# Optimization experiments

Measured on AMD Instinct MI355X. Metric: run time of the kernel, lower is better.

## Reference

```python
import jax, jax.numpy as jnp
import numpy as np

B, C, H, W = 4, 256, 180, 180
N_BOX = 64


def _box_mask(gt_boxes, H, W):
    # gt_boxes: [B, N, 4] int32 = [lt_x, lt_y, rb_x, rb_y]
    # Original fills gt_mask[i, lt_y:rb_y, rb_x:lt_x] = 1 (x-slice is flipped).
    ys = jnp.arange(H)[:, None]            # [H,1]
    xs = jnp.arange(W)[None, :]            # [1,W]
    lt_x = gt_boxes[:, :, 0][:, :, None, None]
    lt_y = gt_boxes[:, :, 1][:, :, None, None]
    rb_x = gt_boxes[:, :, 2][:, :, None, None]
    rb_y = gt_boxes[:, :, 3][:, :, None, None]
    inside = (ys >= lt_y) & (ys < rb_y) & (xs >= rb_x) & (xs < lt_x)  # [B,N,H,W]
    return jnp.any(inside, axis=1)         # [B,H,W] bool


def setup_inputs() -> dict:
    key = jax.random.key(0)
    k1, k2, k3, k4, k5, k6 = jax.random.split(key, 6)
    inp = jax.random.normal(k1, (B, C, H, W), dtype=jnp.float32)
    tgt = jax.random.normal(k2, (B, C, H, W), dtype=jnp.float32)
    # Build boxes with flipped-x convention: lt_x > rb_x, lt_y < rb_y.
    x2 = jax.random.randint(k3, (B, N_BOX), 0, W - 50)
    bw = jax.random.randint(k4, (B, N_BOX), 5, 45)
    y1 = jax.random.randint(k5, (B, N_BOX), 0, H - 50)
    bh = jax.random.randint(k6, (B, N_BOX), 5, 45)
    gt_boxes = jnp.stack([x2 + bw, y1, x2, y1 + bh], axis=-1).astype(jnp.int32)
    return {"input": inp, "target": tgt, "gt_boxes": gt_boxes}


def reference(input, target, gt_boxes):
    b, c, h, w = input.shape
    mask = _box_mask(gt_boxes, h, w)                        # [B,H,W]
    x = jnp.transpose(input, (0, 2, 3, 1))                  # [B,H,W,C]
    t = jnp.transpose(target, (0, 2, 3, 1))
    positives = jnp.any(t != 0, axis=-1).astype(x.dtype) * mask.astype(x.dtype)
    pos_normalizer = jnp.sum(positives)
    reg_weights = positives / pos_normalizer                # [B,H,W]
    # masked weighted MSE; zero weights make non-positive pixels contribute 0,
    # matching the original's boolean-index gather.
    t = jnp.where(jnp.isnan(t), x, t)
    loss = 0.5 * (x - t) ** 2 * reg_weights[..., None]      # [B,H,W,C]
    imitation_loss = jnp.sum(jnp.mean(loss, axis=-1)) / b
    return imitation_loss
```

## Files before the change

### kernel.cpp

```cpp
#include <hip/hip_runtime.h>
#include <hip/hip_bf16.h>

#define B_    4
#define C_    256
#define H_    180
#define W_    180
#define NBOX  64
#define HW_   (H_ * W_)
#define NPIX  (B_ * HW_)

__global__ __launch_bounds__(256) void mask_feat_loss_main(
    const float* __restrict__ x,
    const float* __restrict__ t,
    const int*   __restrict__ boxes,
    float*        ws_sum,
    unsigned int* ws_cnt)
{
    const int p = blockIdx.x * blockDim.x + threadIdx.x;

    float s = 0.0f;
    int   cnt = 0;

    if (p < NPIX) {
        const int b  = p / HW_;
        const int hw = p - b * HW_;
        const int h  = hw / W_;
        const int w  = hw - h * W_;

        bool mask = false;
        const int* bb = boxes + b * NBOX * 4;
        #pragma unroll 8
        for (int n = 0; n < NBOX; ++n) {
            const int ltx = bb[n * 4 + 0];
            const int lty = bb[n * 4 + 1];
            const int rbx = bb[n * 4 + 2];
            const int rby = bb[n * 4 + 3];
            mask |= ((h >= lty) & (h < rby) & (w >= rbx) & (w < ltx));
        }

        if (mask) {
            const float* xp = x + (size_t)b * C_ * HW_ + hw;
            const float* tp = t + (size_t)b * C_ * HW_ + hw;
            bool anynz = false;
            #pragma unroll 8
            for (int c = 0; c < C_; ++c) {
                const float tv = tp[(size_t)c * HW_];
                const float xv = xp[(size_t)c * HW_];
                anynz |= (tv != 0.0f);
                const float d = xv - tv;
                float term = 0.5f * d * d;
                if (isnan(tv)) term = 0.0f;
                s += term;
            }
            if (anynz) cnt = 1;
            else       s = 0.0f;
        }
    }

    #pragma unroll
    for (int off = 32; off > 0; off >>= 1) {
        s   += __shfl_down(s, off, 64);
        cnt += __shfl_down(cnt, off, 64);
    }

    __shared__ float ssum[4];
    __shared__ int   scnt[4];
    const int lane = threadIdx.x & 63;
    const int wid  = threadIdx.x >> 6;
    if (lane == 0) { ssum[wid] = s; scnt[wid] = cnt; }
    __syncthreads();

    if (threadIdx.x == 0) {
        const float S  = ssum[0] + ssum[1] + ssum[2] + ssum[3];
        const int   Cn = scnt[0] + scnt[1] + scnt[2] + scnt[3];
        if (S != 0.0f) atomicAdd(ws_sum, S);
        if (Cn != 0)   atomicAdd(ws_cnt, (unsigned int)Cn);
    }
}

__global__ void mask_feat_loss_finalize(const float* ws_sum,
                                        const unsigned int* ws_cnt,
                                        float* out)
{
    const float S = ws_sum[0];
    const float n = (float)ws_cnt[0];
    out[0] = S / (n * (float)C_ * (float)B_);
}

extern "C" void kernel_launch(void* const* d_in, const int* in_sizes, int n_in,
                              void* d_out, int out_size, void* d_ws, size_t ws_size,
                              hipStream_t stream)
{
    const float* x     = (const float*)d_in[0];
    const float* t     = (const float*)d_in[1];
    const int*   boxes = (const int*)d_in[2];
    float* out = (float*)d_out;

    float*        ws_sum = (float*)d_ws;
    unsigned int* ws_cnt = (unsigned int*)((char*)d_ws + sizeof(float));

    hipMemsetAsync(d_ws, 0, 2 * sizeof(unsigned int), stream);

    const int threads = 256;
    const int blocks  = (NPIX + threads - 1) / threads;
    mask_feat_loss_main<<<blocks, threads, 0, stream>>>(x, t, boxes, ws_sum, ws_cnt);
    mask_feat_loss_finalize<<<1, 1, 0, stream>>>(ws_sum, ws_cnt, out);
}
```

Measured before the change: 54.19 us.

## Split channel loop across four waves per pixel group

```diff
diff --git a/kernel.cpp b/kernel.cpp
--- a/kernel.cpp
+++ b/kernel.cpp
@@ -16,65 +16,66 @@
     float*        ws_sum,
     unsigned int* ws_cnt)
 {
-    const int p = blockIdx.x * blockDim.x + threadIdx.x;
+    const int lane = threadIdx.x & 63;
+    const int wid  = threadIdx.x >> 6;
+    const int p    = blockIdx.x * 64 + lane;
+
+    const int b  = p / HW_;
+    const int hw = p - b * HW_;
+    const int h  = hw / W_;
+    const int w  = hw - h * W_;
+
+    bool mask = false;
+    const int* bb = boxes + b * NBOX * 4;
+    #pragma unroll 8
+    for (int n = 0; n < NBOX; ++n) {
+        const int ltx = bb[n * 4 + 0];
+        const int lty = bb[n * 4 + 1];
+        const int rbx = bb[n * 4 + 2];
+        const int rby = bb[n * 4 + 3];
+        mask |= ((h >= lty) & (h < rby) & (w >= rbx) & (w < ltx));
+    }
 
     float s = 0.0f;
-    int   cnt = 0;
-
-    if (p < NPIX) {
-        const int b  = p / HW_;
-        const int hw = p - b * HW_;
-        const int h  = hw / W_;
-        const int w  = hw - h * W_;
-
-        bool mask = false;
-        const int* bb = boxes + b * NBOX * 4;
+    int   nz = 0;
+    if (mask) {
+        const size_t base = ((size_t)b * C_ + wid * 64) * HW_ + hw;
+        const float* xp = x + base;
+        const float* tp = t + base;
         #pragma unroll 8
-        for (int n = 0; n < NBOX; ++n) {
-            const int ltx = bb[n * 4 + 0];
-            const int lty = bb[n * 4 + 1];
-            const int rbx = bb[n * 4 + 2];
-            const int rby = bb[n * 4 + 3];
-            mask |= ((h >= lty) & (h < rby) & (w >= rbx) & (w < ltx));
-        }
-
-        if (mask) {
-            const float* xp = x + (size_t)b * C_ * HW_ + hw;
-            const float* tp = t + (size_t)b * C_ * HW_ + hw;
-            bool anynz = false;
-            #pragma unroll 8
-            for (int c = 0; c < C_; ++c) {
-                const float tv = tp[(size_t)c * HW_];
-                const float xv = xp[(size_t)c * HW_];
-                anynz |= (tv != 0.0f);
-                const float d = xv - tv;
-                float term = 0.5f * d * d;
-                if (isnan(tv)) term = 0.0f;
-                s += term;
-            }
-            if (anynz) cnt = 1;
-            else       s = 0.0f;
+        for (int c = 0; c < 64; ++c) {
+            const float tv = tp[(size_t)c * HW_];
+            const float xv = xp[(size_t)c * HW_];
+            nz |= (tv != 0.0f);
+            const float d = xv - tv;
+            float term = 0.5f * d * d;
+            if (isnan(tv)) term = 0.0f;
+            s += term;
         }
     }
 
-    #pragma unroll
-    for (int off = 32; off > 0; off >>= 1) {
-        s   += __shfl_down(s, off, 64);
-        cnt += __shfl_down(cnt, off, 64);
-    }
-
-    __shared__ float ssum[4];
-    __shared__ int   scnt[4];
-    const int lane = threadIdx.x & 63;
-    const int wid  = threadIdx.x >> 6;
-    if (lane == 0) { ssum[wid] = s; scnt[wid] = cnt; }
+    __shared__ float ssum[4][64];
+    __shared__ int   snz[4][64];
+    ssum[wid][lane] = s;
+    snz[wid][lane]  = nz;
     __syncthreads();
 
-    if (threadIdx.x == 0) {
-        const float S  = ssum[0] + ssum[1] + ssum[2] + ssum[3];
-        const int   Cn = scnt[0] + scnt[1] + scnt[2] + scnt[3];
-        if (S != 0.0f) atomicAdd(ws_sum, S);
-        if (Cn != 0)   atomicAdd(ws_cnt, (unsigned int)Cn);
+    if (wid == 0) {
+        float s_tot  = ssum[0][lane] + ssum[1][lane] + ssum[2][lane] + ssum[3][lane];
+        int   nz_tot = snz[0][lane] | snz[1][lane] | snz[2][lane] | snz[3][lane];
+
+        float sc = (mask && nz_tot) ? s_tot : 0.0f;
+        int   cc = (mask && nz_tot) ? 1 : 0;
+
+        #pragma unroll
+        for (int off = 32; off > 0; off >>= 1) {
+            sc += __shfl_down(sc, off, 64);
+            cc += __shfl_down(cc, off, 64);
+        }
+        if (lane == 0) {
+            if (sc != 0.0f) atomicAdd(ws_sum, sc);
+            if (cc != 0)    atomicAdd(ws_cnt, (unsigned int)cc);
+        }
     }
 }
 
@@ -102,7 +103,7 @@
     hipMemsetAsync(d_ws, 0, 2 * sizeof(unsigned int), stream);
 
     const int threads = 256;
-    const int blocks  = (NPIX + threads - 1) / threads;
+    const int blocks  = NPIX / 64;
     mask_feat_loss_main<<<blocks, threads, 0, stream>>>(x, t, boxes, ws_sum, ws_cnt);
     mask_feat_loss_finalize<<<1, 1, 0, stream>>>(ws_sum, ws_cnt, out);
 }
```

Measured after the change: 69.47 us. +28.2%, slower.

## Split loss into mask, channel-chunked float4 streaming, gate and final kernels

Applied to the files above, without the earlier changes.

```diff
diff --git a/kernel.cpp b/kernel.cpp
--- a/kernel.cpp
+++ b/kernel.cpp
@@ -7,84 +7,244 @@
 #define W_    180
 #define NBOX  64
 #define HW_   (H_ * W_)
-#define NPIX  (B_ * HW_)
-
-__global__ __launch_bounds__(256) void mask_feat_loss_main(
+#define TILES 127
+#define CCH   16
+#define NBLK  (TILES * B_)
+
+#define WMASK_OFF   0
+#define TILEANY_OFF (WMASK_OFF + B_ * HW_)
+#define PSUM_OFF    130112
+#define PNZ_OFF     (PSUM_OFF + CCH * B_ * HW_ * 4)
+#define BSUM_OFF    (PNZ_OFF + CCH * B_ * HW_)
+#define BCNT_OFF    (BSUM_OFF + NBLK * 4)
+#define WS_NEED     (BCNT_OFF + NBLK * 4)
+
+__global__ __launch_bounds__(256) void mfl_mask(
+    const int* __restrict__ boxes,
+    unsigned char* __restrict__ wmask,
+    unsigned char* __restrict__ tileany)
+{
+    const int tid = threadIdx.x;
+    const int bx  = blockIdx.x;
+    const int b   = blockIdx.y;
+
+    __shared__ int sbox[NBOX * 4];
+    __shared__ int sany;
+    sbox[tid] = boxes[b * NBOX * 4 + tid];
+    if (tid == 0) sany = 0;
+    __syncthreads();
+
+    const int hw = bx * 256 + tid;
+    int msk = 0;
+    if (hw < HW_) {
+        const int h = hw / W_, w = hw - (hw / W_) * W_;
+        #pragma unroll 8
+        for (int n = 0; n < NBOX; ++n) {
+            const int ltx = sbox[n * 4 + 0];
+            const int lty = sbox[n * 4 + 1];
+            const int rbx = sbox[n * 4 + 2];
+            const int rby = sbox[n * 4 + 3];
+            msk |= ((h >= lty) & (h < rby) & (w >= rbx) & (w < ltx));
+        }
+        wmask[b * HW_ + hw] = (unsigned char)msk;
+    }
+    if (msk) sany = 1;
+    __syncthreads();
+    if (tid == 0) tileany[b * TILES + bx] = (unsigned char)sany;
+}
+
+__global__ __launch_bounds__(256) void mfl_stream(
     const float* __restrict__ x,
     const float* __restrict__ t,
-    const int*   __restrict__ boxes,
-    float*        ws_sum,
-    unsigned int* ws_cnt)
+    const unsigned char* __restrict__ tileany,
+    float* __restrict__ psum,
+    unsigned char* __restrict__ pnz)
+{
+    const int tid  = threadIdx.x;
+    const int lane = tid & 63;
+    const int wid  = tid >> 6;
+    const int bx   = blockIdx.x;
+    const int k    = blockIdx.y;
+    const int b    = blockIdx.z;
+
+    if (tileany[b * TILES + bx] == 0) return;
+
+    __shared__ float         ssum[4][256];
+    __shared__ unsigned char snz[4][256];
+
+    float a0 = 0.f, a1 = 0.f, a2 = 0.f, a3 = 0.f;
+    int   n0 = 0, n1 = 0, n2 = 0, n3 = 0;
+
+    const int hw0 = bx * 256 + 4 * lane;
+    if (hw0 < HW_) {
+        const int c0 = k * 16 + wid * 4;
+        const size_t base = ((size_t)(b * C_ + c0)) * HW_ + hw0;
+        const float4* xp = (const float4*)(x + base);
+        const float4* tp = (const float4*)(t + base);
+        const size_t cs = HW_ / 4;
+
+        const float4 tv0 = tp[0];
+        const float4 tv1 = tp[cs];
+        const float4 tv2 = tp[2 * cs];
+        const float4 tv3 = tp[3 * cs];
+        const float4 xv0 = xp[0];
+        const float4 xv1 = xp[cs];
+        const float4 xv2 = xp[2 * cs];
+        const float4 xv3 = xp[3 * cs];
+        __builtin_amdgcn_sched_barrier(0);
+
+        #define CONSUME(tv, xv)                                        \
+        {                                                              \
+            n0 += (tv.x != 0.f); n1 += (tv.y != 0.f);                  \
+            n2 += (tv.z != 0.f); n3 += (tv.w != 0.f);                  \
+            float d0 = xv.x - tv.x, d1 = xv.y - tv.y;                  \
+            float d2 = xv.z - tv.z, d3 = xv.w - tv.w;                  \
+            float s0 = 0.5f * d0 * d0, s1 = 0.5f * d1 * d1;            \
+            float s2 = 0.5f * d2 * d2, s3 = 0.5f * d3 * d3;            \
+            if (isnan(tv.x)) s0 = 0.f;  if (isnan(tv.y)) s1 = 0.f;     \
+            if (isnan(tv.z)) s2 = 0.f;  if (isnan(tv.w)) s3 = 0.f;     \
+            a0 += s0; a1 += s1; a2 += s2; a3 += s3;                    \
+        }
+        CONSUME(tv0, xv0)
+        CONSUME(tv1, xv1)
+        CONSUME(tv2, xv2)
+        CONSUME(tv3, xv3)
+        #undef CONSUME
+    }
+
+    const int pi = 4 * lane;
+    ssum[wid][pi + 0] = a0; ssum[wid][pi + 1] = a1;
+    ssum[wid][pi + 2] = a2; ssum[wid][pi + 3] = a3;
+    snz[wid][pi + 0] = (unsigned char)n0; snz[wid][pi + 1] = (unsigned char)n1;
+    snz[wid][pi + 2] = (unsigned char)n2; snz[wid][pi + 3] = (unsigned char)n3;
+    __syncthreads();
+
+    const int hw = bx * 256 + tid;
+    if (hw < HW_) {
+        const float tot = ssum[0][tid] + ssum[1][tid] + ssum[2][tid] + ssum[3][tid];
+        const int   nzc = snz[0][tid] + snz[1][tid] + snz[2][tid] + snz[3][tid];
+        const size_t plane = (size_t)(k * B_ + b) * HW_;
+        psum[plane + hw] = tot;
+        pnz[plane + hw]  = (unsigned char)nzc;
+    }
+}
+
+__global__ __launch_bounds__(256) void mfl_gate(
+    const float* __restrict__ psum,
+    const unsigned char* __restrict__ pnz,
+    const unsigned char* __restrict__ wmask,
+    float* __restrict__ bsum,
+    unsigned int* __restrict__ bcnt)
+{
+    const int tid = threadIdx.x;
+    const int bx  = blockIdx.x;
+    const int b   = blockIdx.y;
+    const int hw  = bx * 256 + tid;
+
+    float s = 0.f;
+    int   nz = 0;
+    int   msk = 0;
+    if (hw < HW_) {
+        msk = wmask[b * HW_ + hw];
+        if (msk) {
+            #pragma unroll
+            for (int k = 0; k < CCH; ++k) {
+                const size_t idx = (size_t)(k * B_ + b) * HW_ + hw;
+                s  += psum[idx];
+                nz += pnz[idx];
+            }
+        }
+    }
+    const bool ok = msk && (nz > 0);
+    float sc = ok ? s : 0.f;
+    int   cc = ok ? 1 : 0;
+
+    #pragma unroll
+    for (int off = 32; off > 0; off >>= 1) {
+        sc += __shfl_down(sc, off, 64);
+        cc += __shfl_down(cc, off, 64);
+    }
+    __shared__ float ws[4];
+    __shared__ int   wc[4];
+    if ((tid & 63) == 0) { ws[tid >> 6] = sc; wc[tid >> 6] = cc; }
+    __syncthreads();
+    if (tid == 0) {
+        bsum[b * TILES + bx] = ws[0] + ws[1] + ws[2] + ws[3];
+        bcnt[b * TILES + bx] = (unsigned int)(wc[0] + wc[1] + wc[2] + wc[3]);
+    }
+}
+
+__global__ __launch_bounds__(512) void mfl_final(
+    const float* __restrict__ bsum,
+    const unsigned int* __restrict__ bcnt,
+    float* __restrict__ out)
+{
+    const int tid = threadIdx.x;
+    float s = (tid < NBLK) ? bsum[tid] : 0.f;
+    int   c = (tid < NBLK) ? (int)bcnt[tid] : 0;
+    #pragma unroll
+    for (int off = 32; off > 0; off >>= 1) {
+        s += __shfl_down(s, off, 64);
+        c += __shfl_down(c, off, 64);
+    }
+    __shared__ float ws[8];
+    __shared__ int   wc[8];
+    if ((tid & 63) == 0) { ws[tid >> 6] = s; wc[tid >> 6] = c; }
+    __syncthreads();
+    if (tid == 0) {
+        float S = 0.f; int n = 0;
+        #pragma unroll
+        for (int i = 0; i < 8; ++i) { S += ws[i]; n += wc[i]; }
+        out[0] = S / ((float)n * (float)C_ * (float)B_);
+    }
+}
+
+__global__ __launch_bounds__(256) void mfl_fallback(
+    const float* __restrict__ x, const float* __restrict__ t,
+    const int* __restrict__ boxes, float* ws_sum, unsigned int* ws_cnt)
 {
     const int p = blockIdx.x * blockDim.x + threadIdx.x;
-
-    float s = 0.0f;
-    int   cnt = 0;
-
-    if (p < NPIX) {
-        const int b  = p / HW_;
-        const int hw = p - b * HW_;
-        const int h  = hw / W_;
-        const int w  = hw - h * W_;
-
+    float s = 0.0f; int cnt = 0;
+    if (p < B_ * HW_) {
+        const int b = p / HW_, hw = p - b * HW_;
+        const int h = hw / W_, w = hw - h * W_;
         bool mask = false;
         const int* bb = boxes + b * NBOX * 4;
-        #pragma unroll 8
         for (int n = 0; n < NBOX; ++n) {
-            const int ltx = bb[n * 4 + 0];
-            const int lty = bb[n * 4 + 1];
-            const int rbx = bb[n * 4 + 2];
-            const int rby = bb[n * 4 + 3];
-            mask |= ((h >= lty) & (h < rby) & (w >= rbx) & (w < ltx));
-        }
-
+            mask |= ((h >= bb[n*4+1]) & (h < bb[n*4+3]) & (w >= bb[n*4+2]) & (w < bb[n*4+0]));
+        }
         if (mask) {
             const float* xp = x + (size_t)b * C_ * HW_ + hw;
             const float* tp = t + (size_t)b * C_ * HW_ + hw;
             bool anynz = false;
-            #pragma unroll 8
             for (int c = 0; c < C_; ++c) {
-                const float tv = tp[(size_t)c * HW_];
-                const float xv = xp[(size_t)c * HW_];
+                const float tv = tp[(size_t)c * HW_], xv = xp[(size_t)c * HW_];
                 anynz |= (tv != 0.0f);
                 const float d = xv - tv;
                 float term = 0.5f * d * d;
                 if (isnan(tv)) term = 0.0f;
                 s += term;
             }
-            if (anynz) cnt = 1;
-            else       s = 0.0f;
-        }
-    }
-
-    #pragma unroll
+            if (anynz) cnt = 1; else s = 0.0f;
+        }
+    }
     for (int off = 32; off > 0; off >>= 1) {
-        s   += __shfl_down(s, off, 64);
-        cnt += __shfl_down(cnt, off, 64);
-    }
-
-    __shared__ float ssum[4];
-    __shared__ int   scnt[4];
-    const int lane = threadIdx.x & 63;
-    const int wid  = threadIdx.x >> 6;
-    if (lane == 0) { ssum[wid] = s; scnt[wid] = cnt; }
-    __syncthreads();
-
+        s += __shfl_down(s, off, 64); cnt += __shfl_down(cnt, off, 64);
+    }
+    __shared__ float ssum[4]; __shared__ int scnt[4];
+    if ((threadIdx.x & 63) == 0) { ssum[threadIdx.x >> 6] = s; scnt[threadIdx.x >> 6] = cnt; }
+    __syncthreads();
     if (threadIdx.x == 0) {
-        const float S  = ssum[0] + ssum[1] + ssum[2] + ssum[3];
-        const int   Cn = scnt[0] + scnt[1] + scnt[2] + scnt[3];
+        const float S = ssum[0]+ssum[1]+ssum[2]+ssum[3];
+        const int Cn = scnt[0]+scnt[1]+scnt[2]+scnt[3];
         if (S != 0.0f) atomicAdd(ws_sum, S);
-        if (Cn != 0)   atomicAdd(ws_cnt, (unsigned int)Cn);
-    }
-}
-
-__global__ void mask_feat_loss_finalize(const float* ws_sum,
-                                        const unsigned int* ws_cnt,
-                                        float* out)
-{
-    const float S = ws_sum[0];
-    const float n = (float)ws_cnt[0];
-    out[0] = S / (n * (float)C_ * (float)B_);
+        if (Cn != 0) atomicAdd(ws_cnt, (unsigned int)Cn);
+    }
+}
+
+__global__ void mfl_fallback_final(const float* ws_sum, const unsigned int* ws_cnt, float* out)
+{
+    out[0] = ws_sum[0] / ((float)ws_cnt[0] * (float)C_ * (float)B_);
 }
 
 extern "C" void kernel_launch(void* const* d_in, const int* in_sizes, int n_in,
@@ -95,14 +255,32 @@
     const float* t     = (const float*)d_in[1];
     const int*   boxes = (const int*)d_in[2];
     float* out = (float*)d_out;
-
-    float*        ws_sum = (float*)d_ws;
-    unsigned int* ws_cnt = (unsigned int*)((char*)d_ws + sizeof(float));
-
-    hipMemsetAsync(d_ws, 0, 2 * sizeof(unsigned int), stream);
-
-    const int threads = 256;
-    const int blocks  = (NPIX + threads - 1) / threads;
-    mask_feat_loss_main<<<blocks, threads, 0, stream>>>(x, t, boxes, ws_sum, ws_cnt);
-    mask_feat_loss_finalize<<<1, 1, 0, stream>>>(ws_sum, ws_cnt, out);
-}
+    char* ws = (char*)d_ws;
+
+    if (ws_size < (size_t)WS_NEED) {
+        float* ws_sum = (float*)ws;
+        unsigned int* ws_cnt = (unsigned int*)(ws + 4);
+        hipMemsetAsync(d_ws, 0, 8, stream);
+        mfl_fallback<<<(B_ * HW_ + 255) / 256, 256, 0, stream>>>(x, t, boxes, ws_sum, ws_cnt);
+        mfl_fallback_final<<<1, 1, 0, stream>>>(ws_sum, ws_cnt, out);
+        return;
+    }
+
+    unsigned char* wmask   = (unsigned char*)(ws + WMASK_OFF);
+    unsigned char* tileany = (unsigned char*)(ws + TILEANY_OFF);
+    float*         psum    = (float*)(ws + PSUM_OFF);
+    unsigned char* pnz     = (unsigned char*)(ws + PNZ_OFF);
+    float*         bsum    = (float*)(ws + BSUM_OFF);
+    unsigned int*  bcnt    = (unsigned int*)(ws + BCNT_OFF);
+
+    dim3 gm(TILES, B_);
+    mfl_mask<<<gm, 256, 0, stream>>>(boxes, wmask, tileany);
+
+    dim3 ga(TILES, CCH, B_);
+    mfl_stream<<<ga, 256, 0, stream>>>(x, t, tileany, psum, pnz);
+
+    dim3 gb(TILES, B_);
+    mfl_gate<<<gb, 256, 0, stream>>>(psum, pnz, wmask, bsum, bcnt);
+
+    mfl_final<<<1, 512, 0, stream>>>(bsum, bcnt, out);
+}
```

Result: slower. 55.76 us (+2.9%).

## Split loss into mask, channel-chunked float4 streaming, and gate reduction kernels

Applied to the files above, without the earlier changes.

```diff
diff --git a/kernel.cpp b/kernel.cpp
--- a/kernel.cpp
+++ b/kernel.cpp
@@ -1,90 +1,190 @@
 #include <hip/hip_runtime.h>
 #include <hip/hip_bf16.h>
 
-#define B_    4
-#define C_    256
-#define H_    180
-#define W_    180
-#define NBOX  64
-#define HW_   (H_ * W_)
-#define NPIX  (B_ * HW_)
-
-__global__ __launch_bounds__(256) void mask_feat_loss_main(
-    const float* __restrict__ x,
-    const float* __restrict__ t,
-    const int*   __restrict__ boxes,
-    float*        ws_sum,
-    unsigned int* ws_cnt)
+#define B_     4
+#define C_     256
+#define H_     180
+#define W_     180
+#define NBOX   64
+#define HW_    (H_ * W_)
+#define GROUPS (HW_ / 4)
+#define GTILES 32
+#define PTILES 127
+#define KCH    16
+#define CPC    16
+#define NBLK   (PTILES * B_)
+
+#define WMASK_OFF 0
+#define PSUM_OFF  (B_ * HW_)
+#define PNZ_OFF   (PSUM_OFF + KCH * B_ * GROUPS * 16)
+#define ACC_OFF   (PNZ_OFF + KCH * B_ * GROUPS * 4)
+#define WS_NEED   (ACC_OFF + 8)
+
+__global__ __launch_bounds__(256) void mfl_mask(
+    const int* __restrict__ boxes,
+    unsigned char* __restrict__ wmask)
+{
+    const int tid = threadIdx.x;
+    const int bx  = blockIdx.x;
+    const int b   = blockIdx.y;
+
+    __shared__ int sbox[NBOX * 4];
+    sbox[tid] = boxes[b * NBOX * 4 + tid];
+    __syncthreads();
+
+    const int hw = bx * 256 + tid;
+    if (hw < HW_) {
+        const int h = hw / W_, w = hw - (hw / W_) * W_;
+        int msk = 0;
+        #pragma unroll 8
+        for (int n = 0; n < NBOX; ++n) {
+            const int ltx = sbox[n * 4 + 0];
+            const int lty = sbox[n * 4 + 1];
+            const int rbx = sbox[n * 4 + 2];
+            const int rby = sbox[n * 4 + 3];
+            msk |= ((h >= lty) & (h < rby) & (w >= rbx) & (w < ltx));
+        }
+        wmask[b * HW_ + hw] = (unsigned char)msk;
+    }
+}
+
+__global__ __launch_bounds__(256, 8) void mfl_stream(
+    const float4* __restrict__ x4,
+    const float4* __restrict__ t4,
+    const unsigned char* __restrict__ wmask,
+    float4* __restrict__ psum,
+    unsigned int* __restrict__ pnz)
+{
+    const int g = blockIdx.x * 256 + threadIdx.x;
+    if (g >= GROUPS) return;
+    const int k = blockIdx.y;
+    const int b = blockIdx.z;
+
+    const uchar4 m4 = *(const uchar4*)(wmask + b * HW_ + 4 * g);
+    if ((m4.x | m4.y | m4.z | m4.w) == 0) return;
+
+    const size_t fbase = ((size_t)(b * C_ + k * CPC)) * GROUPS + g;
+    const float4* xp = x4 + fbase;
+    const float4* tp = t4 + fbase;
+
+    float a0 = 0.f, a1 = 0.f, a2 = 0.f, a3 = 0.f;
+    int   n0 = 0, n1 = 0, n2 = 0, n3 = 0;
+
+    #pragma unroll 4
+    for (int c = 0; c < CPC; ++c) {
+        const float4 tv = tp[(size_t)c * GROUPS];
+        const float4 xv = xp[(size_t)c * GROUPS];
+        n0 |= (tv.x != 0.f); n1 |= (tv.y != 0.f);
+        n2 |= (tv.z != 0.f); n3 |= (tv.w != 0.f);
+        float d0 = xv.x - tv.x, d1 = xv.y - tv.y;
+        float d2 = xv.z - tv.z, d3 = xv.w - tv.w;
+        float s0 = 0.5f * d0 * d0, s1 = 0.5f * d1 * d1;
+        float s2 = 0.5f * d2 * d2, s3 = 0.5f * d3 * d3;
+        if (isnan(tv.x)) s0 = 0.f;  if (isnan(tv.y)) s1 = 0.f;
+        if (isnan(tv.z)) s2 = 0.f;  if (isnan(tv.w)) s3 = 0.f;
+        a0 += s0; a1 += s1; a2 += s2; a3 += s3;
+    }
+
+    const size_t o = ((size_t)(k * B_ + b)) * GROUPS + g;
+    psum[o] = make_float4(a0, a1, a2, a3);
+    pnz[o]  = (unsigned int)n0 | ((unsigned int)n1 << 8)
+            | ((unsigned int)n2 << 16) | ((unsigned int)n3 << 24);
+}
+
+__global__ __launch_bounds__(256) void mfl_gate(
+    const float* __restrict__ psumf,
+    const unsigned char* __restrict__ pnzb,
+    const unsigned char* __restrict__ wmask,
+    float* __restrict__ ws_sum,
+    unsigned int* __restrict__ ws_cnt)
+{
+    const int tid = threadIdx.x;
+    const int bx  = blockIdx.x;
+    const int b   = blockIdx.y;
+    const int hw  = bx * 256 + tid;
+
+    float s = 0.f;
+    int   nz = 0, msk = 0;
+    if (hw < HW_) {
+        msk = wmask[b * HW_ + hw];
+        if (msk) {
+            const int g = hw >> 2, e = hw & 3;
+            #pragma unroll
+            for (int k = 0; k < KCH; ++k) {
+                const size_t o = ((size_t)(k * B_ + b)) * GROUPS + g;
+                s  += psumf[o * 4 + e];
+                nz |= pnzb[o * 4 + e];
+            }
+        }
+    }
+    const bool ok = msk && nz;
+    float sc = ok ? s : 0.f;
+    int   cc = ok ? 1 : 0;
+
+    #pragma unroll
+    for (int off = 32; off > 0; off >>= 1) {
+        sc += __shfl_down(sc, off, 64);
+        cc += __shfl_down(cc, off, 64);
+    }
+    __shared__ float ws[4];
+    __shared__ int   wc[4];
+    if ((tid & 63) == 0) { ws[tid >> 6] = sc; wc[tid >> 6] = cc; }
+    __syncthreads();
+    if (tid == 0) {
+        const float S  = ws[0] + ws[1] + ws[2] + ws[3];
+        const int   Cn = wc[0] + wc[1] + wc[2] + wc[3];
+        if (S != 0.f) atomicAdd(ws_sum, S);
+        if (Cn != 0)  atomicAdd(ws_cnt, (unsigned int)Cn);
+    }
+}
+
+__global__ void mfl_final(const float* ws_sum, const unsigned int* ws_cnt,
+                          float* out)
+{
+    out[0] = ws_sum[0] / ((float)ws_cnt[0] * (float)C_ * (float)B_);
+}
+
+__global__ __launch_bounds__(256) void mfl_fallback(
+    const float* __restrict__ x, const float* __restrict__ t,
+    const int* __restrict__ boxes, float* ws_sum, unsigned int* ws_cnt)
 {
     const int p = blockIdx.x * blockDim.x + threadIdx.x;
-
-    float s = 0.0f;
-    int   cnt = 0;
-
-    if (p < NPIX) {
-        const int b  = p / HW_;
-        const int hw = p - b * HW_;
-        const int h  = hw / W_;
-        const int w  = hw - h * W_;
-
+    float s = 0.0f; int cnt = 0;
+    if (p < B_ * HW_) {
+        const int b = p / HW_, hw = p - b * HW_;
+        const int h = hw / W_, w = hw - h * W_;
         bool mask = false;
         const int* bb = boxes + b * NBOX * 4;
-        #pragma unroll 8
         for (int n = 0; n < NBOX; ++n) {
-            const int ltx = bb[n * 4 + 0];
-            const int lty = bb[n * 4 + 1];
-            const int rbx = bb[n * 4 + 2];
-            const int rby = bb[n * 4 + 3];
-            mask |= ((h >= lty) & (h < rby) & (w >= rbx) & (w < ltx));
-        }
-
+            mask |= ((h >= bb[n*4+1]) & (h < bb[n*4+3]) & (w >= bb[n*4+2]) & (w < bb[n*4+0]));
+        }
         if (mask) {
             const float* xp = x + (size_t)b * C_ * HW_ + hw;
             const float* tp = t + (size_t)b * C_ * HW_ + hw;
             bool anynz = false;
-            #pragma unroll 8
             for (int c = 0; c < C_; ++c) {
-                const float tv = tp[(size_t)c * HW_];
-                const float xv = xp[(size_t)c * HW_];
+                const float tv = tp[(size_t)c * HW_], xv = xp[(size_t)c * HW_];
                 anynz |= (tv != 0.0f);
                 const float d = xv - tv;
                 float term = 0.5f * d * d;
                 if (isnan(tv)) term = 0.0f;
                 s += term;
             }
-            if (anynz) cnt = 1;
-            else       s = 0.0f;
-        }
-    }
-
-    #pragma unroll
+            if (anynz) cnt = 1; else s = 0.0f;
+        }
+    }
     for (int off = 32; off > 0; off >>= 1) {
-        s   += __shfl_down(s, off, 64);
-        cnt += __shfl_down(cnt, off, 64);
-    }
-
-    __shared__ float ssum[4];
-    __shared__ int   scnt[4];
-    const int lane = threadIdx.x & 63;
-    const int wid  = threadIdx.x >> 6;
-    if (lane == 0) { ssum[wid] = s; scnt[wid] = cnt; }
+        s += __shfl_down(s, off, 64); cnt += __shfl_down(cnt, off, 64);
+    }
+    __shared__ float ssum[4]; __shared__ int scnt[4];
+    if ((threadIdx.x & 63) == 0) { ssum[threadIdx.x >> 6] = s; scnt[threadIdx.x >> 6] = cnt; }
     __syncthreads();
-
     if (threadIdx.x == 0) {
-        const float S  = ssum[0] + ssum[1] + ssum[2] + ssum[3];
-        const int   Cn = scnt[0] + scnt[1] + scnt[2] + scnt[3];
+        const float S = ssum[0]+ssum[1]+ssum[2]+ssum[3];
+        const int Cn = scnt[0]+scnt[1]+scnt[2]+scnt[3];
         if (S != 0.0f) atomicAdd(ws_sum, S);
-        if (Cn != 0)   atomicAdd(ws_cnt, (unsigned int)Cn);
-    }
-}
-
-__global__ void mask_feat_loss_finalize(const float* ws_sum,
-                                        const unsigned int* ws_cnt,
-                                        float* out)
-{
-    const float S = ws_sum[0];
-    const float n = (float)ws_cnt[0];
-    out[0] = S / (n * (float)C_ * (float)B_);
+        if (Cn != 0) atomicAdd(ws_cnt, (unsigned int)Cn);
+    }
 }
 
 extern "C" void kernel_launch(void* const* d_in, const int* in_sizes, int n_in,
@@ -95,14 +195,36 @@
     const float* t     = (const float*)d_in[1];
     const int*   boxes = (const int*)d_in[2];
     float* out = (float*)d_out;
-
-    float*        ws_sum = (float*)d_ws;
-    unsigned int* ws_cnt = (unsigned int*)((char*)d_ws + sizeof(float));
-
-    hipMemsetAsync(d_ws, 0, 2 * sizeof(unsigned int), stream);
-
-    const int threads = 256;
-    const int blocks  = (NPIX + threads - 1) / threads;
-    mask_feat_loss_main<<<blocks, threads, 0, stream>>>(x, t, boxes, ws_sum, ws_cnt);
-    mask_feat_loss_finalize<<<1, 1, 0, stream>>>(ws_sum, ws_cnt, out);
-}
+    char*  ws  = (char*)d_ws;
+
+    if (ws_size < (size_t)WS_NEED) {
+        float* ws_sum = (float*)ws;
+        unsigned int* ws_cnt = (unsigned int*)(ws + 4);
+        hipMemsetAsync(d_ws, 0, 8, stream);
+        mfl_fallback<<<(B_ * HW_ + 255) / 256, 256, 0, stream>>>(x, t, boxes, ws_sum, ws_cnt);
+        mfl_final<<<1, 1, 0, stream>>>(ws_sum, ws_cnt, out);
+        return;
+    }
+
+    unsigned char* wmask  = (unsigned char*)(ws + WMASK_OFF);
+    float4*        psum   = (float4*)(ws + PSUM_OFF);
+    unsigned int*  pnz    = (unsigned int*)(ws + PNZ_OFF);
+    float*         ws_sum = (float*)(ws + ACC_OFF);
+    unsigned int*  ws_cnt = (unsigned int*)(ws + ACC_OFF + 4);
+
+    hipMemsetAsync(ws + ACC_OFF, 0, 8, stream);
+
+    dim3 gm(PTILES, B_);
+    mfl_mask<<<gm, 256, 0, stream>>>(boxes, wmask);
+
+    dim3 ga(GTILES, KCH, B_);
+    mfl_stream<<<ga, 256, 0, stream>>>((const float4*)x, (const float4*)t,
+                                       wmask, psum, pnz);
+
+    dim3 gb(PTILES, B_);
+    mfl_gate<<<gb, 256, 0, stream>>>((const float*)psum,
+                                     (const unsigned char*)pnz,
+                                     wmask, ws_sum, ws_cnt);
+
+    mfl_final<<<1, 1, 0, stream>>>(ws_sum, ws_cnt, out);
+}
```

Result: slower. 61.98 us (+14.4%).
